# Kernel tuning notes

Hardware: AMD Instinct MI355X
Metric: run time of the kernel (lower is better)

The kernel has to match this reference:

```python
import jax, jax.numpy as jnp
import numpy as np

NUM_HEAD = 4
NEG_SLOPE_ATT = 0.2   # GATConv leaky relu slope
NEG_SLOPE_ACT = 0.5   # inter-layer LeakyReLU slope
EPS = 1e-16           # PyG softmax denominator eps


def _leaky_relu(v, slope):
    return jnp.where(v >= 0, v, slope * v)


def gat_conv(h_in, edge_index, W, b, att, bias):
    """Faithful port of GATConv.forward (no edge_attr).
    h_in: [N, in_dim]; edge_index: [2, E] (row 0 = source j, row 1 = target i).
    Adds self loops, computes per-edge attention with leaky-relu, segment softmax
    grouped by edge_index[0] (as in the source), scatter-adds to targets.
    """
    N = h_in.shape[0]
    loops = jnp.arange(N, dtype=edge_index.dtype)
    src = jnp.concatenate([edge_index[0], loops])
    dst = jnp.concatenate([edge_index[1], loops])

    h = (h_in @ W + b).reshape(N, NUM_HEAD, -1)  # [N, H, k]
    x_j = h[src]   # [Ee, H, k] messages from source
    x_i = h[dst]   # [Ee, H, k] target features

    # alpha = sum over 2k of cat([x_i, x_j]) * att ; att: [1, H, 2k]
    k = h.shape[-1]
    alpha = (x_i * att[:, :, :k]).sum(-1) + (x_j * att[:, :, k:]).sum(-1)  # [Ee, H]
    alpha = _leaky_relu(alpha, NEG_SLOPE_ATT)

    # segment softmax grouped by SOURCE node (quirk of original code)
    amax = jax.ops.segment_max(alpha, src, num_segments=N)
    ex = jnp.exp(alpha - amax[src])
    denom = jax.ops.segment_sum(ex, src, num_segments=N)
    alpha = ex / (denom[src] + EPS)

    msg = x_j * alpha[:, :, None]                       # [Ee, H, k]
    out = jax.ops.segment_sum(msg, dst, num_segments=N)  # aggregate at target
    out = out.reshape(N, -1) + bias
    return jax.nn.relu(out)


def setup_inputs() -> dict:
    key = jax.random.key(0)
    ks = jax.random.split(key, 16)
    N, D_IN, D_T, D_H, D_E, C, E = 100000, 256, 128, 128, 128, 3, 1600000

    def glorot(k, shape):
        fan = shape[0] + shape[-1] if len(shape) == 2 else shape[1] * shape[2] + 1
        s = jnp.sqrt(6.0 / fan)
        return jax.random.uniform(k, shape, jnp.float32, -s, s)

    inp = {
        "x": jax.random.normal(ks[0], (N, D_IN), jnp.float32),
        "edge_index": jax.random.randint(ks[1], (2, E), 0, N, jnp.int64)
            if jax.config.jax_enable_x64 else jax.random.randint(ks[1], (2, E), 0, N, jnp.int32),
        "node_index": jax.random.randint(ks[2], (50000,), 0, N, jnp.int32),
        "pheno_W": glorot(ks[3], (D_IN, D_T)),
        "pheno_b": jnp.zeros((D_T,), jnp.float32),
        "W1": glorot(ks[4], (D_T, D_H)), "b1": jnp.zeros((D_H,), jnp.float32),
        "att1": glorot(ks[5], (1, NUM_HEAD, 2 * D_H // NUM_HEAD)),
        "bias1": jnp.zeros((D_H,), jnp.float32),
        "W2": glorot(ks[6], (D_H, D_H)), "b2": jnp.zeros((D_H,), jnp.float32),
        "att2": glorot(ks[7], (1, NUM_HEAD, 2 * D_H // NUM_HEAD)),
        "bias2": jnp.zeros((D_H,), jnp.float32),
        "W3": glorot(ks[8], (D_H, D_E)), "b3": jnp.zeros((D_E,), jnp.float32),
        "att3": glorot(ks[9], (1, NUM_HEAD, 2 * D_E // NUM_HEAD)),
        "bias3": jnp.zeros((D_E,), jnp.float32),
        "out_W": glorot(ks[10], (D_E, C)),
    }
    return inp


def reference(x, edge_index, node_index, pheno_W, pheno_b,
              W1, b1, att1, bias1, W2, b2, att2, bias2, W3, b3, att3, bias3,
              out_W):
    # graph_opt == 'subject' path of GIG_GAT.forward
    g = x @ pheno_W + pheno_b                         # pheno_transform
    g = _leaky_relu(gat_conv(g, edge_index, W1, b1, att1, bias1), NEG_SLOPE_ACT)
    g = _leaky_relu(gat_conv(g, edge_index, W2, b2, att2, bias2), NEG_SLOPE_ACT)
    g = _leaky_relu(gat_conv(g, edge_index, W3, b3, att3, bias3), NEG_SLOPE_ACT)
    x_embed = g
    output = g @ out_W                                # self.out (no bias)
    node_output = output[node_index]
    ypred = jnp.argmax(output, axis=1)
    y_nodepred = ypred[node_index]
    return x_embed, node_output, ypred, y_nodepred
```

## Files before the change

kernel.cpp:

```cpp
#include <hip/hip_runtime.h>
#include <math.h>


#define LRELU_ATT(v) ((v) >= 0.f ? (v) : 0.2f * (v))
#define SCAT_CHUNK 8192

template <int K>
__global__ __launch_bounds__(256)
void gemm_tile(const float* __restrict__ X, const float* __restrict__ W,
               const float* __restrict__ bvec, float* __restrict__ Y, int N)
{
    __shared__ __align__(16) float xt[32][132];
    __shared__ __align__(16) float ws[32][132];

    const int t  = threadIdx.x;
    const int tx = t & 15, ty = t >> 4;
    const int r0 = blockIdx.x * 128;

    float acc[8][8];
#pragma unroll
    for (int i = 0; i < 8; ++i)
#pragma unroll
        for (int j = 0; j < 8; ++j) acc[i][j] = 0.f;

    const int srow = t >> 3;
    const int sk4  = (t & 7) * 4;
    const int wkr  = t >> 5;
    const int wc4  = (t & 31) * 4;

    for (int kc = 0; kc < K; kc += 32) {
#pragma unroll
        for (int p = 0; p < 4; ++p) {
            const int r  = srow + p * 32;
            const int gr = r0 + r;
            float4 v = make_float4(0.f, 0.f, 0.f, 0.f);
            if (gr < N) v = *reinterpret_cast<const float4*>(&X[(size_t)gr * K + kc + sk4]);
            xt[sk4 + 0][r] = v.x; xt[sk4 + 1][r] = v.y;
            xt[sk4 + 2][r] = v.z; xt[sk4 + 3][r] = v.w;
        }
#pragma unroll
        for (int p = 0; p < 4; ++p) {
            const int k = wkr + p * 8;
            float4 v = *reinterpret_cast<const float4*>(&W[(size_t)(kc + k) * 128 + wc4]);
            *reinterpret_cast<float4*>(&ws[k][wc4]) = v;
        }
        __syncthreads();

#pragma unroll
        for (int k = 0; k < 32; ++k) {
            const float4 a0 = *reinterpret_cast<const float4*>(&xt[k][8 * ty]);
            const float4 a1 = *reinterpret_cast<const float4*>(&xt[k][8 * ty + 4]);
            const float4 b0 = *reinterpret_cast<const float4*>(&ws[k][8 * tx]);
            const float4 b1 = *reinterpret_cast<const float4*>(&ws[k][8 * tx + 4]);
            const float av[8] = {a0.x, a0.y, a0.z, a0.w, a1.x, a1.y, a1.z, a1.w};
            const float bv[8] = {b0.x, b0.y, b0.z, b0.w, b1.x, b1.y, b1.z, b1.w};
#pragma unroll
            for (int i = 0; i < 8; ++i)
#pragma unroll
                for (int j = 0; j < 8; ++j)
                    acc[i][j] = fmaf(av[i], bv[j], acc[i][j]);
        }
        __syncthreads();
    }

    const float4 bb0 = *reinterpret_cast<const float4*>(&bvec[8 * tx]);
    const float4 bb1 = *reinterpret_cast<const float4*>(&bvec[8 * tx + 4]);
#pragma unroll
    for (int i = 0; i < 8; ++i) {
        const int gr = r0 + 8 * ty + i;
        if (gr < N) {
            float4 o0 = make_float4(acc[i][0] + bb0.x, acc[i][1] + bb0.y,
                                    acc[i][2] + bb0.z, acc[i][3] + bb0.w);
            float4 o1 = make_float4(acc[i][4] + bb1.x, acc[i][5] + bb1.y,
                                    acc[i][6] + bb1.z, acc[i][7] + bb1.w);
            *reinterpret_cast<float4*>(&Y[(size_t)gr * 128 + 8 * tx])     = o0;
            *reinterpret_cast<float4*>(&Y[(size_t)gr * 128 + 8 * tx + 4]) = o1;
        }
    }
}

__global__ __launch_bounds__(256)
void node_dots(const float* __restrict__ H, const float* __restrict__ att,
               float* __restrict__ ai, float4* __restrict__ pk, int N)
{
    const int lane = threadIdx.x & 63;
    const int n    = blockIdx.x * 4 + (threadIdx.x >> 6);
    if (n >= N) return;

    const float v0 = H[(size_t)n * 128 + lane];
    const float v1 = H[(size_t)n * 128 + 64 + lane];
    const int hh = lane >> 5, k = lane & 31;

    float si0 = v0 * att[hh * 64 + k];
    float sj0 = v0 * att[hh * 64 + 32 + k];
    float si1 = v1 * att[(2 + hh) * 64 + k];
    float sj1 = v1 * att[(2 + hh) * 64 + 32 + k];

#pragma unroll
    for (int m = 1; m < 32; m <<= 1) {
        si0 += __shfl_xor(si0, m);
        sj0 += __shfl_xor(sj0, m);
        si1 += __shfl_xor(si1, m);
        sj1 += __shfl_xor(sj1, m);
    }
    if ((lane & 31) == 0) {
        const int hA = lane >> 5;
        ai[(size_t)n * 4 + hA]     = si0;
        ai[(size_t)n * 4 + 2 + hA] = si1;
        ((float*)&pk[(size_t)n * 4 + hA])[0]     = sj0;
        ((float*)&pk[(size_t)n * 4 + 2 + hA])[0] = sj1;
    }
}

__global__ __launch_bounds__(256)
void count_deg(const int* __restrict__ ei, int E, int N,
               int* __restrict__ cnt_s, int* __restrict__ cnt_d)
{
    const int e = blockIdx.x * 256 + threadIdx.x;
    if (e >= E + N) return;
    int s, d;
    if (e < E) { s = ei[e]; d = ei[E + e]; } else { s = d = e - E; }
    atomicAdd(&cnt_s[s], 1);
    atomicAdd(&cnt_d[d], 1);
}

__global__ __launch_bounds__(256)
void scan_part(const int* __restrict__ cnt, int* __restrict__ bsum, int n)
{
    __shared__ int sm[256];
    const int i = blockIdx.x * 256 + threadIdx.x;
    sm[threadIdx.x] = (i < n) ? cnt[i] : 0;
    __syncthreads();
    for (int s = 128; s > 0; s >>= 1) {
        if (threadIdx.x < s) sm[threadIdx.x] += sm[threadIdx.x + s];
        __syncthreads();
    }
    if (threadIdx.x == 0) bsum[blockIdx.x] = sm[0];
}

__global__ __launch_bounds__(1024)
void scan_bsums(int* __restrict__ bsum, int nb)
{
    __shared__ int sm[1024];
    const int i = threadIdx.x;
    if (i < nb) sm[i] = bsum[i];
    __syncthreads();
    if (i == 0) {
        int run = 0;
        for (int t = 0; t < nb; ++t) { int v = sm[t]; sm[t] = run; run += v; }
    }
    __syncthreads();
    if (i < nb) bsum[i] = sm[i];
}

__global__ __launch_bounds__(256)
void scan_final(const int* __restrict__ cnt, const int* __restrict__ bsum,
                int* __restrict__ row, int n)
{
    const int i = blockIdx.x * 256 + threadIdx.x;
    const int lane = threadIdx.x & 63, wid = threadIdx.x >> 6;
    int v = (i < n) ? cnt[i] : 0;
    int inc = v;
#pragma unroll
    for (int d = 1; d < 64; d <<= 1) {
        int y = __shfl_up(inc, d);
        if (lane >= d) inc += y;
    }
    __shared__ int wsum[4];
    if (lane == 63) wsum[wid] = inc;
    __syncthreads();
    int wofs = 0;
    for (int w = 0; w < wid; ++w) wofs += wsum[w];
    if (i < n) row[i] = inc - v + wofs + bsum[blockIdx.x];
}

__global__ __launch_bounds__(256)
void init_tails(const int* __restrict__ row_s, const int* __restrict__ row_d,
                int* __restrict__ tail_s, int* __restrict__ tail_d, int NB)
{
    const int b = blockIdx.x * 256 + threadIdx.x;
    if (b >= NB) return;
    tail_s[b] = row_s[b << 8];
    tail_d[b] = row_d[b << 8];
}

__global__ __launch_bounds__(256)
void radix_scatter(const int* __restrict__ ei, int E, int N, int NB,
                   int* __restrict__ tail_s, int* __restrict__ tail_d,
                   int* __restrict__ bufs, int* __restrict__ bufd)
{
    __shared__ int cnt_s[512], cnt_d[512];
    const int base_e = blockIdx.x * SCAT_CHUNK;
    const int end_e  = min(base_e + SCAT_CHUNK, E + N);

    for (int i = threadIdx.x; i < NB; i += 256) { cnt_s[i] = 0; cnt_d[i] = 0; }
    __syncthreads();

    for (int e = base_e + threadIdx.x; e < end_e; e += 256) {
        int s, d;
        if (e < E) { s = ei[e]; d = ei[E + e]; } else { s = d = e - E; }
        atomicAdd(&cnt_s[s >> 8], 1);
        atomicAdd(&cnt_d[d >> 8], 1);
    }
    __syncthreads();

    for (int b = threadIdx.x; b < NB; b += 256) {
        const int c0 = cnt_s[b];
        cnt_s[b] = c0 ? atomicAdd(&tail_s[b], c0) : 0;
        const int c1 = cnt_d[b];
        cnt_d[b] = c1 ? atomicAdd(&tail_d[b], c1) : 0;
    }
    __syncthreads();

    for (int e = base_e + threadIdx.x; e < end_e; e += 256) {
        int s, d;
        if (e < E) { s = ei[e]; d = ei[E + e]; } else { s = d = e - E; }
        const int ps = atomicAdd(&cnt_s[s >> 8], 1);
        bufs[ps] = ((s & 255) << 17) | d;
        const int pd = atomicAdd(&cnt_d[d >> 8], 1);
        bufd[pd] = ((d & 255) << 17) | s;
    }
}

__global__ __launch_bounds__(256)
void bucket_place(const int* __restrict__ row_s, int* __restrict__ ent_s, const int* __restrict__ bufs,
                  const int* __restrict__ row_d, int* __restrict__ ent_d, const int* __restrict__ bufd,
                  int N, int NB, int EN)
{
    const int* __restrict__ row = (blockIdx.y == 0) ? row_s : row_d;
    int*       __restrict__ ent = (blockIdx.y == 0) ? ent_s : ent_d;
    const int* __restrict__ buf = (blockIdx.y == 0) ? bufs  : bufd;

    __shared__ int fc[256];
    const int node0 = blockIdx.x << 8;
    const int start = row[node0];
    const int nxt   = node0 + 256;
    const int end   = (nxt >= N) ? EN : row[nxt];

    fc[threadIdx.x] = 0;
    __syncthreads();

    for (int i = start + threadIdx.x; i < end; i += 256) {
        const unsigned w  = (unsigned)buf[i];
        const int loc  = (int)(w >> 17);
        const int slot = atomicAdd(&fc[loc], 1);
        ent[row[node0 | loc] + slot] = (int)(w & 0x1FFFFu);
    }
}

__global__ __launch_bounds__(256)
void sort_rows_wave(const int* __restrict__ row, int* __restrict__ ent, int N, int EN)
{
    const int lane = threadIdx.x & 63;
    const int n    = blockIdx.x * 4 + (threadIdx.x >> 6);
    if (n >= N) return;
    const int lo  = row[n];
    const int hi  = (n == N - 1) ? EN : row[n + 1];
    const int deg = hi - lo;

    if (deg > 64) {
        if (lane == 0) {
            for (int i = lo + 1; i < hi; ++i) {
                int v = ent[i], j = i - 1;
                while (j >= lo && ent[j] > v) { ent[j + 1] = ent[j]; --j; }
                ent[j + 1] = v;
            }
        }
        return;
    }

    int v = (lane < deg) ? ent[lo + lane] : 0x7FFFFFFF;
#pragma unroll
    for (int k = 2; k <= 64; k <<= 1) {
#pragma unroll
        for (int j = k >> 1; j > 0; j >>= 1) {
            const int w  = __shfl_xor(v, j);
            const bool up   = ((lane & k) == 0);
            const bool lowr = ((lane & j) == 0);
            v = (lowr == up) ? min(v, w) : max(v, w);
        }
    }
    if (lane < deg) ent[lo + lane] = v;
}

__global__ __launch_bounds__(256)
void softmax_src(const int* __restrict__ row_s, const int* __restrict__ ent_s,
                 const float* __restrict__ ai, float4* __restrict__ pk, int N, int EN)
{
    const int lane = threadIdx.x & 63;
    const int n    = blockIdx.x * 4 + (threadIdx.x >> 6);
    if (n >= N) return;
    const int row = row_s[n];
    const int end = (n == N - 1) ? EN : row_s[n + 1];
    const int deg = end - row;
    const int slot = lane & 15, h = lane >> 4;
    const float ajh = ((const float*)&pk[(size_t)n * 4 + h])[0];

    float m, ssum;
    if (deg <= 64) {
        float a0 = -INFINITY, a1 = -INFINITY, a2 = -INFINITY, a3 = -INFINITY;
        int t = row + slot;
        if (t < end) { a0 = LRELU_ATT(ai[(size_t)ent_s[t] * 4 + h] + ajh); t += 16; }
        if (t < end) { a1 = LRELU_ATT(ai[(size_t)ent_s[t] * 4 + h] + ajh); t += 16; }
        if (t < end) { a2 = LRELU_ATT(ai[(size_t)ent_s[t] * 4 + h] + ajh); t += 16; }
        if (t < end) { a3 = LRELU_ATT(ai[(size_t)ent_s[t] * 4 + h] + ajh); }
        m = fmaxf(fmaxf(a0, a1), fmaxf(a2, a3));
#pragma unroll
        for (int mm = 1; mm < 16; mm <<= 1) m = fmaxf(m, __shfl_xor(m, mm));
        ssum = __expf(a0 - m);
        ssum += __expf(a1 - m);
        ssum += __expf(a2 - m);
        ssum += __expf(a3 - m);
#pragma unroll
        for (int mm = 1; mm < 16; mm <<= 1) ssum += __shfl_xor(ssum, mm);
    } else {
        m = -INFINITY;
        for (int t = row + slot; t < end; t += 16) {
            const int d = ent_s[t];
            const float a = LRELU_ATT(ai[(size_t)d * 4 + h] + ajh);
            m = fmaxf(m, a);
        }
#pragma unroll
        for (int mm = 1; mm < 16; mm <<= 1) m = fmaxf(m, __shfl_xor(m, mm));
        ssum = 0.f;
        for (int t = row + slot; t < end; t += 16) {
            const int d = ent_s[t];
            const float a = LRELU_ATT(ai[(size_t)d * 4 + h] + ajh);
            ssum += __expf(a - m);
        }
#pragma unroll
        for (int mm = 1; mm < 16; mm <<= 1) ssum += __shfl_xor(ssum, mm);
    }

    if (slot == 0) {
        float* p = (float*)&pk[(size_t)n * 4 + h];
        p[1] = m;
        p[2] = 1.f / (ssum + 1e-16f);
    }
}

__global__ __launch_bounds__(256)
void aggregate_dst(const int* __restrict__ row_d, const int* __restrict__ ent_d,
                   const float* __restrict__ ai, const float4* __restrict__ pk,
                   const float* __restrict__ H, const float* __restrict__ bias,
                   float* __restrict__ OUT, int N, int EN)
{
    const int lane = threadIdx.x & 63;
    const int half = lane >> 5, ll = lane & 31;
    const int n    = blockIdx.x * 8 + (threadIdx.x >> 6) * 2 + half;
    if (n >= N) return;
    const int row = row_d[n];
    const int end = (n == N - 1) ? EN : row_d[n + 1];
    const int h   = ll >> 3;
    const float aih = ai[(size_t)n * 4 + h];

    float4 acc = make_float4(0.f, 0.f, 0.f, 0.f);
    int t = row;
    for (; t + 4 <= end; t += 4) {
        const int s0 = ent_d[t + 0];
        const int s1 = ent_d[t + 1];
        const int s2 = ent_d[t + 2];
        const int s3 = ent_d[t + 3];

        const float4 h0 = *reinterpret_cast<const float4*>(&H[(size_t)s0 * 128 + ll * 4]);
        const float4 h1 = *reinterpret_cast<const float4*>(&H[(size_t)s1 * 128 + ll * 4]);
        const float4 h2 = *reinterpret_cast<const float4*>(&H[(size_t)s2 * 128 + ll * 4]);
        const float4 h3 = *reinterpret_cast<const float4*>(&H[(size_t)s3 * 128 + ll * 4]);

        const float4 p0 = pk[(size_t)s0 * 4 + h];
        const float4 p1 = pk[(size_t)s1 * 4 + h];
        const float4 p2 = pk[(size_t)s2 * 4 + h];
        const float4 p3 = pk[(size_t)s3 * 4 + h];

        const float c0 = __expf(LRELU_ATT(aih + p0.x) - p0.y) * p0.z;
        const float c1 = __expf(LRELU_ATT(aih + p1.x) - p1.y) * p1.z;
        const float c2 = __expf(LRELU_ATT(aih + p2.x) - p2.y) * p2.z;
        const float c3 = __expf(LRELU_ATT(aih + p3.x) - p3.y) * p3.z;

        acc.x = fmaf(h0.x, c0, acc.x); acc.y = fmaf(h0.y, c0, acc.y);
        acc.z = fmaf(h0.z, c0, acc.z); acc.w = fmaf(h0.w, c0, acc.w);
        acc.x = fmaf(h1.x, c1, acc.x); acc.y = fmaf(h1.y, c1, acc.y);
        acc.z = fmaf(h1.z, c1, acc.z); acc.w = fmaf(h1.w, c1, acc.w);
        acc.x = fmaf(h2.x, c2, acc.x); acc.y = fmaf(h2.y, c2, acc.y);
        acc.z = fmaf(h2.z, c2, acc.z); acc.w = fmaf(h2.w, c2, acc.w);
        acc.x = fmaf(h3.x, c3, acc.x); acc.y = fmaf(h3.y, c3, acc.y);
        acc.z = fmaf(h3.z, c3, acc.z); acc.w = fmaf(h3.w, c3, acc.w);
    }
    for (; t < end; ++t) {
        const int s = ent_d[t];
        const float4 hv = *reinterpret_cast<const float4*>(&H[(size_t)s * 128 + ll * 4]);
        const float4 pv = pk[(size_t)s * 4 + h];
        const float c   = __expf(LRELU_ATT(aih + pv.x) - pv.y) * pv.z;
        acc.x = fmaf(hv.x, c, acc.x); acc.y = fmaf(hv.y, c, acc.y);
        acc.z = fmaf(hv.z, c, acc.z); acc.w = fmaf(hv.w, c, acc.w);
    }
    const float4 bv = *reinterpret_cast<const float4*>(&bias[ll * 4]);
    float4 o;
    o.x = fmaxf(acc.x + bv.x, 0.f);
    o.y = fmaxf(acc.y + bv.y, 0.f);
    o.z = fmaxf(acc.z + bv.z, 0.f);
    o.w = fmaxf(acc.w + bv.w, 0.f);
    *reinterpret_cast<float4*>(&OUT[(size_t)n * 128 + ll * 4]) = o;
}

__global__ __launch_bounds__(256)
void out_kernel(const float* __restrict__ G, const float* __restrict__ oW,
                float* __restrict__ out3, float* __restrict__ ypredF, int N)
{
    __shared__ float w[384];
    for (int i = threadIdx.x; i < 384; i += 256) w[i] = oW[i];
    __syncthreads();
    const int n = blockIdx.x * 256 + threadIdx.x;
    if (n >= N) return;
    const float* g = G + (size_t)n * 128;
    float a0 = 0.f, a1 = 0.f, a2 = 0.f;
    for (int k = 0; k < 128; k += 4) {
        float4 gv = *reinterpret_cast<const float4*>(&g[k]);
        a0 = fmaf(gv.x, w[(k+0)*3+0], a0); a1 = fmaf(gv.x, w[(k+0)*3+1], a1); a2 = fmaf(gv.x, w[(k+0)*3+2], a2);
        a0 = fmaf(gv.y, w[(k+1)*3+0], a0); a1 = fmaf(gv.y, w[(k+1)*3+1], a1); a2 = fmaf(gv.y, w[(k+1)*3+2], a2);
        a0 = fmaf(gv.z, w[(k+2)*3+0], a0); a1 = fmaf(gv.z, w[(k+2)*3+1], a1); a2 = fmaf(gv.z, w[(k+2)*3+2], a2);
        a0 = fmaf(gv.w, w[(k+3)*3+0], a0); a1 = fmaf(gv.w, w[(k+3)*3+1], a1); a2 = fmaf(gv.w, w[(k+3)*3+2], a2);
    }
    out3[(size_t)n * 3 + 0] = a0;
    out3[(size_t)n * 3 + 1] = a1;
    out3[(size_t)n * 3 + 2] = a2;
    int idx = 0; float best = a0;
    if (a1 > best) { best = a1; idx = 1; }
    if (a2 > best) { best = a2; idx = 2; }
    ypredF[n] = (float)idx;
}

__global__ __launch_bounds__(256)
void gather_kernel(const int* __restrict__ nix, const float* __restrict__ out3,
                   const float* __restrict__ ypredF, float* __restrict__ nodeOut,
                   float* __restrict__ ynode, int M)
{
    const int i = blockIdx.x * 256 + threadIdx.x;
    if (i >= M) return;
    const int n = nix[i];
    nodeOut[(size_t)i * 3 + 0] = out3[(size_t)n * 3 + 0];
    nodeOut[(size_t)i * 3 + 1] = out3[(size_t)n * 3 + 1];
    nodeOut[(size_t)i * 3 + 2] = out3[(size_t)n * 3 + 2];
    ynode[i] = ypredF[n];
}

extern "C" void kernel_launch(void* const* d_in, const int* in_sizes, int n_in,
                              void* d_out, int out_size, void* d_ws, size_t ws_size,
                              hipStream_t stream)
{
    const float* x      = (const float*)d_in[0];
    const int*   ei     = (const int*)d_in[1];
    const int*   nodeix = (const int*)d_in[2];
    const float* phW    = (const float*)d_in[3];
    const float* phb    = (const float*)d_in[4];
    const float* Wl[3]   = {(const float*)d_in[5],  (const float*)d_in[9],  (const float*)d_in[13]};
    const float* bl[3]   = {(const float*)d_in[6],  (const float*)d_in[10], (const float*)d_in[14]};
    const float* attl[3] = {(const float*)d_in[7],  (const float*)d_in[11], (const float*)d_in[15]};
    const float* bsl[3]  = {(const float*)d_in[8],  (const float*)d_in[12], (const float*)d_in[16]};
    const float* outW    = (const float*)d_in[17];

    const int N  = in_sizes[0] / 256;
    const int E  = in_sizes[1] / 2;
    const int M  = in_sizes[2];
    const int EN = E + N;
    const int NB = (N + 255) >> 8;

    float*  P     = (float*)d_ws;
    float*  Q     = P + (size_t)N * 128;
    float*  ai    = Q + (size_t)N * 128;
    float4* pk    = (float4*)(ai + (size_t)N * 4);
    float*  out3  = (float*)(pk + (size_t)N * 4);
    int* row_s   = (int*)(out3 + (size_t)N * 3);
    int* row_d   = row_s + N;
    int* cnt_s   = row_d + N;
    int* cnt_d   = cnt_s + N;
    int* tail_s  = cnt_d + N;
    int* tail_d  = tail_s + NB;
    int* bsum_s  = tail_d + NB;
    int* bsum_d  = bsum_s + 1024;
    int* ent_s   = bsum_d + 1024;
    int* ent_d   = ent_s + (size_t)EN;

    int* bufA_s = (int*)Q;
    int* bufA_d = bufA_s + (size_t)EN;

    float* o_embed   = (float*)d_out;
    float* o_nodeout = o_embed + (size_t)N * 128;
    float* o_ypred   = o_nodeout + (size_t)M * 3;
    float* o_ynode   = o_ypred + N;

    const int nb = (N + 255) / 256;
    const int ng = (N + 127) / 128;

    hipMemsetAsync(cnt_s, 0, (size_t)2 * N * sizeof(int), stream);
    count_deg<<<(EN + 255) / 256, 256, 0, stream>>>(ei, E, N, cnt_s, cnt_d);
    scan_part<<<nb, 256, 0, stream>>>(cnt_s, bsum_s, N);
    scan_part<<<nb, 256, 0, stream>>>(cnt_d, bsum_d, N);
    scan_bsums<<<1, 1024, 0, stream>>>(bsum_s, nb);
    scan_bsums<<<1, 1024, 0, stream>>>(bsum_d, nb);
    scan_final<<<nb, 256, 0, stream>>>(cnt_s, bsum_s, row_s, N);
    scan_final<<<nb, 256, 0, stream>>>(cnt_d, bsum_d, row_d, N);
    init_tails<<<(NB + 255) / 256, 256, 0, stream>>>(row_s, row_d, tail_s, tail_d, NB);
    radix_scatter<<<(EN + SCAT_CHUNK - 1) / SCAT_CHUNK, 256, 0, stream>>>(
        ei, E, N, NB, tail_s, tail_d, bufA_s, bufA_d);
    bucket_place<<<dim3(NB, 2), 256, 0, stream>>>(row_s, ent_s, bufA_s,
                                                  row_d, ent_d, bufA_d, N, NB, EN);
    sort_rows_wave<<<(N + 3) / 4, 256, 0, stream>>>(row_s, ent_s, N, EN);
    sort_rows_wave<<<(N + 3) / 4, 256, 0, stream>>>(row_d, ent_d, N, EN);

    gemm_tile<256><<<ng, 256, 0, stream>>>(x, phW, phb, P, N);

    for (int l = 0; l < 3; ++l) {
        float* tgt = (l == 2) ? o_embed : P;
        gemm_tile<128><<<ng, 256, 0, stream>>>(P, Wl[l], bl[l], Q, N);
        node_dots<<<(N + 3) / 4, 256, 0, stream>>>(Q, attl[l], ai, pk, N);
        softmax_src<<<(N + 3) / 4, 256, 0, stream>>>(row_s, ent_s, ai, pk, N, EN);
        aggregate_dst<<<(N + 7) / 8, 256, 0, stream>>>(row_d, ent_d, ai, pk,
                                                       Q, bsl[l], tgt, N, EN);
    }

    out_kernel<<<(N + 255) / 256, 256, 0, stream>>>(o_embed, outW, out3, o_ypred, N);
    gather_kernel<<<(M + 255) / 256, 256, 0, stream>>>(nodeix, out3, o_ypred, o_nodeout, o_ynode, M);
}
```

Baseline: 1.166 ms.

## Fuse attention dots into GEMM epilogue and merge paired CSR-build kernels

```diff
diff --git a/kernel.cpp b/kernel.cpp
--- a/kernel.cpp
+++ b/kernel.cpp
@@ -5,10 +5,12 @@
 #define LRELU_ATT(v) ((v) >= 0.f ? (v) : 0.2f * (v))
 #define SCAT_CHUNK 8192
 
-template <int K>
+template <int K, bool DOTS>
 __global__ __launch_bounds__(256)
 void gemm_tile(const float* __restrict__ X, const float* __restrict__ W,
-               const float* __restrict__ bvec, float* __restrict__ Y, int N)
+               const float* __restrict__ bvec, float* __restrict__ Y,
+               const float* __restrict__ att, float* __restrict__ ai,
+               float4* __restrict__ pk, int N)
 {
     __shared__ __align__(16) float xt[32][132];
     __shared__ __align__(16) float ws[32][132];
@@ -65,50 +67,40 @@
 
     const float4 bb0 = *reinterpret_cast<const float4*>(&bvec[8 * tx]);
     const float4 bb1 = *reinterpret_cast<const float4*>(&bvec[8 * tx + 4]);
+
+    const int h  = tx >> 2;
+    const int k0 = (8 * tx) & 31;
+    float4 ati0, ati1, atj0, atj1;
+    if (DOTS) {
+        ati0 = *reinterpret_cast<const float4*>(&att[h * 64 + k0]);
+        ati1 = *reinterpret_cast<const float4*>(&att[h * 64 + k0 + 4]);
+        atj0 = *reinterpret_cast<const float4*>(&att[h * 64 + 32 + k0]);
+        atj1 = *reinterpret_cast<const float4*>(&att[h * 64 + 32 + k0 + 4]);
+    }
+
 #pragma unroll
     for (int i = 0; i < 8; ++i) {
         const int gr = r0 + 8 * ty + i;
+        float4 o0 = make_float4(acc[i][0] + bb0.x, acc[i][1] + bb0.y,
+                                acc[i][2] + bb0.z, acc[i][3] + bb0.w);
+        float4 o1 = make_float4(acc[i][4] + bb1.x, acc[i][5] + bb1.y,
+                                acc[i][6] + bb1.z, acc[i][7] + bb1.w);
         if (gr < N) {
-            float4 o0 = make_float4(acc[i][0] + bb0.x, acc[i][1] + bb0.y,
-                                    acc[i][2] + bb0.z, acc[i][3] + bb0.w);
-            float4 o1 = make_float4(acc[i][4] + bb1.x, acc[i][5] + bb1.y,
-                                    acc[i][6] + bb1.z, acc[i][7] + bb1.w);
             *reinterpret_cast<float4*>(&Y[(size_t)gr * 128 + 8 * tx])     = o0;
             *reinterpret_cast<float4*>(&Y[(size_t)gr * 128 + 8 * tx + 4]) = o1;
         }
-    }
-}
-
-__global__ __launch_bounds__(256)
-void node_dots(const float* __restrict__ H, const float* __restrict__ att,
-               float* __restrict__ ai, float4* __restrict__ pk, int N)
-{
-    const int lane = threadIdx.x & 63;
-    const int n    = blockIdx.x * 4 + (threadIdx.x >> 6);
-    if (n >= N) return;
-
-    const float v0 = H[(size_t)n * 128 + lane];
-    const float v1 = H[(size_t)n * 128 + 64 + lane];
-    const int hh = lane >> 5, k = lane & 31;
-
-    float si0 = v0 * att[hh * 64 + k];
-    float sj0 = v0 * att[hh * 64 + 32 + k];
-    float si1 = v1 * att[(2 + hh) * 64 + k];
-    float sj1 = v1 * att[(2 + hh) * 64 + 32 + k];
-
-#pragma unroll
-    for (int m = 1; m < 32; m <<= 1) {
-        si0 += __shfl_xor(si0, m);
-        sj0 += __shfl_xor(sj0, m);
-        si1 += __shfl_xor(si1, m);
-        sj1 += __shfl_xor(sj1, m);
-    }
-    if ((lane & 31) == 0) {
-        const int hA = lane >> 5;
-        ai[(size_t)n * 4 + hA]     = si0;
-        ai[(size_t)n * 4 + 2 + hA] = si1;
-        ((float*)&pk[(size_t)n * 4 + hA])[0]     = sj0;
-        ((float*)&pk[(size_t)n * 4 + 2 + hA])[0] = sj1;
+        if (DOTS) {
+            float pi = o0.x * ati0.x + o0.y * ati0.y + o0.z * ati0.z + o0.w * ati0.w
+                     + o1.x * ati1.x + o1.y * ati1.y + o1.z * ati1.z + o1.w * ati1.w;
+            float pj = o0.x * atj0.x + o0.y * atj0.y + o0.z * atj0.z + o0.w * atj0.w
+                     + o1.x * atj1.x + o1.y * atj1.y + o1.z * atj1.z + o1.w * atj1.w;
+            pi += __shfl_xor(pi, 1); pi += __shfl_xor(pi, 2);
+            pj += __shfl_xor(pj, 1); pj += __shfl_xor(pj, 2);
+            if ((tx & 3) == 0 && gr < N) {
+                ai[(size_t)gr * 4 + h] = pi;
+                ((float*)&pk[(size_t)gr * 4 + h])[0] = pj;
+            }
+        }
     }
 }
 
@@ -125,8 +117,11 @@
 }
 
 __global__ __launch_bounds__(256)
-void scan_part(const int* __restrict__ cnt, int* __restrict__ bsum, int n)
-{
+void scan_part2(const int* __restrict__ cnt_s, const int* __restrict__ cnt_d,
+                int* __restrict__ bsum_s, int* __restrict__ bsum_d, int n)
+{
+    const int* cnt = blockIdx.y ? cnt_d : cnt_s;
+    int* bsum      = blockIdx.y ? bsum_d : bsum_s;
     __shared__ int sm[256];
     const int i = blockIdx.x * 256 + threadIdx.x;
     sm[threadIdx.x] = (i < n) ? cnt[i] : 0;
@@ -139,8 +134,9 @@
 }
 
 __global__ __launch_bounds__(1024)
-void scan_bsums(int* __restrict__ bsum, int nb)
-{
+void scan_bsums2(int* __restrict__ bsum_s, int* __restrict__ bsum_d, int nb)
+{
+    int* bsum = blockIdx.y ? bsum_d : bsum_s;
     __shared__ int sm[1024];
     const int i = threadIdx.x;
     if (i < nb) sm[i] = bsum[i];
@@ -154,9 +150,16 @@
 }
 
 __global__ __launch_bounds__(256)
-void scan_final(const int* __restrict__ cnt, const int* __restrict__ bsum,
-                int* __restrict__ row, int n)
-{
+void scan_final2(const int* __restrict__ cnt_s, const int* __restrict__ cnt_d,
+                 const int* __restrict__ bsum_s, const int* __restrict__ bsum_d,
+                 int* __restrict__ row_s, int* __restrict__ row_d,
+                 int* __restrict__ tail_s, int* __restrict__ tail_d, int n)
+{
+    const int* cnt  = blockIdx.y ? cnt_d  : cnt_s;
+    const int* bsum = blockIdx.y ? bsum_d : bsum_s;
+    int* row        = blockIdx.y ? row_d  : row_s;
+    int* tail       = blockIdx.y ? tail_d : tail_s;
+
     const int i = blockIdx.x * 256 + threadIdx.x;
     const int lane = threadIdx.x & 63, wid = threadIdx.x >> 6;
     int v = (i < n) ? cnt[i] : 0;
@@ -171,17 +174,11 @@
     __syncthreads();
     int wofs = 0;
     for (int w = 0; w < wid; ++w) wofs += wsum[w];
-    if (i < n) row[i] = inc - v + wofs + bsum[blockIdx.x];
-}
-
-__global__ __launch_bounds__(256)
-void init_tails(const int* __restrict__ row_s, const int* __restrict__ row_d,
-                int* __restrict__ tail_s, int* __restrict__ tail_d, int NB)
-{
-    const int b = blockIdx.x * 256 + threadIdx.x;
-    if (b >= NB) return;
-    tail_s[b] = row_s[b << 8];
-    tail_d[b] = row_d[b << 8];
+    if (i < n) {
+        const int r = inc - v + wofs + bsum[blockIdx.x];
+        row[i] = r;
+        if ((i & 255) == 0) tail[i >> 8] = r;
+    }
 }
 
 __global__ __launch_bounds__(256)
@@ -249,8 +246,13 @@
 }
 
 __global__ __launch_bounds__(256)
-void sort_rows_wave(const int* __restrict__ row, int* __restrict__ ent, int N, int EN)
-{
+void sort_rows_wave2(const int* __restrict__ row_s, int* __restrict__ ent_s,
+                     const int* __restrict__ row_d, int* __restrict__ ent_d,
+                     int N, int EN)
+{
+    const int* row = blockIdx.y ? row_d : row_s;
+    int*       ent = blockIdx.y ? ent_d : ent_s;
+
     const int lane = threadIdx.x & 63;
     const int n    = blockIdx.x * 4 + (threadIdx.x >> 6);
     if (n >= N) return;
@@ -356,21 +358,27 @@
 
     float4 acc = make_float4(0.f, 0.f, 0.f, 0.f);
     int t = row;
+    const int astart = min((row + 3) & ~3, end);
+    for (; t < astart; ++t) {
+        const int s = ent_d[t];
+        const float4 hv = *reinterpret_cast<const float4*>(&H[(size_t)s * 128 + ll * 4]);
+        const float4 pv = pk[(size_t)s * 4 + h];
+        const float c   = __expf(LRELU_ATT(aih + pv.x) - pv.y) * pv.z;
+        acc.x = fmaf(hv.x, c, acc.x); acc.y = fmaf(hv.y, c, acc.y);
+        acc.z = fmaf(hv.z, c, acc.z); acc.w = fmaf(hv.w, c, acc.w);
+    }
     for (; t + 4 <= end; t += 4) {
-        const int s0 = ent_d[t + 0];
-        const int s1 = ent_d[t + 1];
-        const int s2 = ent_d[t + 2];
-        const int s3 = ent_d[t + 3];
-
-        const float4 h0 = *reinterpret_cast<const float4*>(&H[(size_t)s0 * 128 + ll * 4]);
-        const float4 h1 = *reinterpret_cast<const float4*>(&H[(size_t)s1 * 128 + ll * 4]);
-        const float4 h2 = *reinterpret_cast<const float4*>(&H[(size_t)s2 * 128 + ll * 4]);
-        const float4 h3 = *reinterpret_cast<const float4*>(&H[(size_t)s3 * 128 + ll * 4]);
-
-        const float4 p0 = pk[(size_t)s0 * 4 + h];
-        const float4 p1 = pk[(size_t)s1 * 4 + h];
-        const float4 p2 = pk[(size_t)s2 * 4 + h];
-        const float4 p3 = pk[(size_t)s3 * 4 + h];
+        const int4 sv = *reinterpret_cast<const int4*>(&ent_d[t]);
+
+        const float4 h0 = *reinterpret_cast<const float4*>(&H[(size_t)sv.x * 128 + ll * 4]);
+        const float4 h1 = *reinterpret_cast<const float4*>(&H[(size_t)sv.y * 128 + ll * 4]);
+        const float4 h2 = *reinterpret_cast<const float4*>(&H[(size_t)sv.z * 128 + ll * 4]);
+        const float4 h3 = *reinterpret_cast<const float4*>(&H[(size_t)sv.w * 128 + ll * 4]);
+
+        const float4 p0 = pk[(size_t)sv.x * 4 + h];
+        const float4 p1 = pk[(size_t)sv.y * 4 + h];
+        const float4 p2 = pk[(size_t)sv.z * 4 + h];
+        const float4 p3 = pk[(size_t)sv.w * 4 + h];
 
         const float c0 = __expf(LRELU_ATT(aih + p0.x) - p0.y) * p0.z;
         const float c1 = __expf(LRELU_ATT(aih + p1.x) - p1.y) * p1.z;
@@ -463,20 +471,21 @@
     const int E  = in_sizes[1] / 2;
     const int M  = in_sizes[2];
     const int EN = E + N;
-    const int NB = (N + 255) >> 8;
+    const int NB  = (N + 255) >> 8;
+    const int NB4 = (NB + 3) & ~3;
 
     float*  P     = (float*)d_ws;
     float*  Q     = P + (size_t)N * 128;
     float*  ai    = Q + (size_t)N * 128;
     float4* pk    = (float4*)(ai + (size_t)N * 4);
     float*  out3  = (float*)(pk + (size_t)N * 4);
-    int* row_s   = (int*)(out3 + (size_t)N * 3);
+    int* row_s   = (int*)(out3 + (size_t)N * 4);
     int* row_d   = row_s + N;
     int* cnt_s   = row_d + N;
     int* cnt_d   = cnt_s + N;
     int* tail_s  = cnt_d + N;
-    int* tail_d  = tail_s + NB;
-    int* bsum_s  = tail_d + NB;
+    int* tail_d  = tail_s + NB4;
+    int* bsum_s  = tail_d + NB4;
     int* bsum_d  = bsum_s + 1024;
     int* ent_s   = bsum_d + 1024;
     int* ent_d   = ent_s + (size_t)EN;
@@ -494,26 +503,21 @@
 
     hipMemsetAsync(cnt_s, 0, (size_t)2 * N * sizeof(int), stream);
     count_deg<<<(EN + 255) / 256, 256, 0, stream>>>(ei, E, N, cnt_s, cnt_d);
-    scan_part<<<nb, 256, 0, stream>>>(cnt_s, bsum_s, N);
-    scan_part<<<nb, 256, 0, stream>>>(cnt_d, bsum_d, N);
-    scan_bsums<<<1, 1024, 0, stream>>>(bsum_s, nb);
-    scan_bsums<<<1, 1024, 0, stream>>>(bsum_d, nb);
-    scan_final<<<nb, 256, 0, stream>>>(cnt_s, bsum_s, row_s, N);
-    scan_final<<<nb, 256, 0, stream>>>(cnt_d, bsum_d, row_d, N);
-    init_tails<<<(NB + 255) / 256, 256, 0, stream>>>(row_s, row_d, tail_s, tail_d, NB);
+    scan_part2<<<dim3(nb, 2), 256, 0, stream>>>(cnt_s, cnt_d, bsum_s, bsum_d, N);
+    scan_bsums2<<<dim3(1, 2), 1024, 0, stream>>>(bsum_s, bsum_d, nb);
+    scan_final2<<<dim3(nb, 2), 256, 0, stream>>>(cnt_s, cnt_d, bsum_s, bsum_d,
+                                                 row_s, row_d, tail_s, tail_d, N);
     radix_scatter<<<(EN + SCAT_CHUNK - 1) / SCAT_CHUNK, 256, 0, stream>>>(
         ei, E, N, NB, tail_s, tail_d, bufA_s, bufA_d);
     bucket_place<<<dim3(NB, 2), 256, 0, stream>>>(row_s, ent_s, bufA_s,
                                                   row_d, ent_d, bufA_d, N, NB, EN);
-    sort_rows_wave<<<(N + 3) / 4, 256, 0, stream>>>(row_s, ent_s, N, EN);
-    sort_rows_wave<<<(N + 3) / 4, 256, 0, stream>>>(row_d, ent_d, N, EN);
-
-    gemm_tile<256><<<ng, 256, 0, stream>>>(x, phW, phb, P, N);
+    sort_rows_wave2<<<dim3((N + 3) / 4, 2), 256, 0, stream>>>(row_s, ent_s, row_d, ent_d, N, EN);
+
+    gemm_tile<256, false><<<ng, 256, 0, stream>>>(x, phW, phb, P, nullptr, nullptr, nullptr, N);
 
     for (int l = 0; l < 3; ++l) {
         float* tgt = (l == 2) ? o_embed : P;
-        gemm_tile<128><<<ng, 256, 0, stream>>>(P, Wl[l], bl[l], Q, N);
-        node_dots<<<(N + 3) / 4, 256, 0, stream>>>(Q, attl[l], ai, pk, N);
+        gemm_tile<128, true><<<ng, 256, 0, stream>>>(P, Wl[l], bl[l], Q, attl[l], ai, pk, N);
         softmax_src<<<(N + 3) / 4, 256, 0, stream>>>(row_s, ent_s, ai, pk, N, EN);
         aggregate_dst<<<(N + 7) / 8, 256, 0, stream>>>(row_d, ent_d, ai, pk,
                                                        Q, bsl[l], tgt, N, EN);
```

Measured after the change: 1.099 ms. 1.06x faster.
